# Kernel optimization log

Measured on AMD Instinct MI355X. Metric: run time of the kernel, lower is better.

The kernel has to match this reference:

```python
import jax, jax.numpy as jnp
import numpy as np

BLANK = 0
SIZE_AVERAGE = True


def rnnt_loss(acts, labels, act_lens, label_lens):
    # acts: (B, T, U+1, V) raw logits; warp-transducer applies log_softmax internally
    B, T, U1, V = acts.shape
    U = U1 - 1
    logp = jax.nn.log_softmax(acts, axis=-1)          # (B,T,U1,V)
    lp_blank = logp[..., BLANK]                       # (B,T,U1)
    # emission log-prob of label u at grid point (t,u): logp[b,t,u,labels[b,u]]
    lp_emit = jnp.take_along_axis(
        logp[:, :, :U, :], labels[:, None, :, None].astype(jnp.int32), axis=3
    )[..., 0]                                         # (B,T,U)

    # alpha[0,0]=0 ; alpha[0,u] = sum_{k<u} emit[0,k]
    row0 = jnp.concatenate(
        [jnp.zeros((B, 1), acts.dtype), jnp.cumsum(lp_emit[:, 0, :], axis=1)], axis=1
    )                                                 # (B,U1)

    def outer(prev_row, xs):
        blank_prev, emit_t = xs                       # (B,U1), (B,U)
        fb = prev_row + blank_prev                    # arrive via blank from t-1
        def inner(carry, x):
            fb_u, em_prev = x                         # (B,), (B,)
            a = jnp.logaddexp(fb_u, carry + em_prev)  # blank vs emit path
            return a, a
        _, rest = jax.lax.scan(inner, fb[:, 0], (fb[:, 1:].T, emit_t.T))  # (U,B)
        row = jnp.concatenate([fb[:, :1], rest.T], axis=1)               # (B,U1)
        return row, row

    xs = (jnp.moveaxis(lp_blank[:, :-1, :], 1, 0),   # (T-1,B,U1)
          jnp.moveaxis(lp_emit[:, 1:, :], 1, 0))     # (T-1,B,U)
    _, rows = jax.lax.scan(outer, row0, xs)          # (T-1,B,U1)
    alpha = jnp.concatenate([row0[None], rows], axis=0)  # (T,B,U1)

    b_idx = jnp.arange(B)
    t_idx = act_lens.astype(jnp.int32) - 1
    u_idx = label_lens.astype(jnp.int32)
    loglike = alpha[t_idx, b_idx, u_idx] + lp_blank[b_idx, t_idx, u_idx]
    total = -jnp.sum(loglike)
    if SIZE_AVERAGE:
        total = total / B
    return total.reshape(1)


def setup_inputs() -> dict:
    key = jax.random.key(0)
    k1, k2, k3, k4 = jax.random.split(key, 4)
    B, T, U, V = 8, 256, 100, 128
    acts = jax.random.normal(k1, (B, T, U + 1, V), dtype=jnp.float32)
    labels = jax.random.randint(k2, (B, U), 0, V, dtype=jnp.int64)
    act_lens = jax.random.randint(k3, (B,), T // 2, T + 1, dtype=jnp.int32)
    label_lens = jax.random.randint(k4, (B,), U // 2, U + 1, dtype=jnp.int32)
    return {"acts": acts, "labels": labels, "act_lens": act_lens, "label_lens": label_lens}


def reference(acts, labels, act_lens, label_lens):
    return rnnt_loss(acts, labels, act_lens, label_lens)
```

## Files before the change

### kernel.cpp

```cpp
#include <hip/hip_runtime.h>
#include <math.h>


#define B_DIM  8
#define T_DIM  256
#define U_DIM  100
#define U1_DIM 101
#define V_DIM  128

#define ROWU   128
#define DROWS  360
#define NEGF   (-8.0e29f)
#define LOG2E  1.4426950408889634f
#define LN2    0.69314718055994530942f

#define NITMAX 88
#define VROWU  320
#define DEPTH  16

typedef unsigned uv2 __attribute__((ext_vector_type(2)));

__device__ __forceinline__ float ubit(unsigned u) { return __builtin_bit_cast(float, u); }
__device__ __forceinline__ float logadd2(float a, float b) {
    float m = fmaxf(a, b);
    float e = exp2f(-fabsf(a - b));
    return m + log2f(1.0f + e);
}
__device__ __forceinline__ float lse3(float a, float b, float c) {
    float m = fmaxf(fmaxf(a, b), c);
    float s = exp2f(a - m) + exp2f(b - m) + exp2f(c - m);
    return m + log2f(s);
}
__device__ __forceinline__ float lse5(float a, float b, float c, float d, float e) {
    float m = fmaxf(fmaxf(fmaxf(a, b), c), fmaxf(d, e));
    float s = exp2f(a - m) + exp2f(b - m) + exp2f(c - m) + exp2f(d - m) + exp2f(e - m);
    return m + log2f(s);
}
__device__ __forceinline__ float lane_shr1(float x) {
    int r = __builtin_amdgcn_update_dpp(0, __builtin_bit_cast(int, x),
                                        0x138 , 0xF, 0xF, true);
    return __builtin_bit_cast(float, r);
}
__device__ __forceinline__ unsigned f2bf(float f) {
    unsigned u = __builtin_bit_cast(unsigned, f);
    u += 0x7FFF + ((u >> 16) & 1);
    return u >> 16;
}

struct W2 { float tA, mA, lA, tB, mB, lB; };
__device__ __forceinline__ W2 buildW2m(uv2 c0, uv2 cm, int l, int d, int tl, int ul) {
    const int ua = 2 * l, ub = 2 * l + 1;
    float BL0a = ubit(c0.x << 16), EM0a = ubit(c0.x & 0xFFFF0000u);
    float BL0b = ubit(c0.y << 16), EM0b = ubit(c0.y & 0xFFFF0000u);
    float BLma = ubit(cm.x << 16), EMma = ubit(cm.x & 0xFFFF0000u);
    float BLmb = ubit(cm.y << 16), EMmb = ubit(cm.y & 0xFFFF0000u);
    BL0a = (ua <= ul && (unsigned)(d - 1 - ua) <= (unsigned)tl) ? BL0a : NEGF;
    BL0b = (ub <= ul && (unsigned)(d - 1 - ub) <= (unsigned)tl) ? BL0b : NEGF;
    EM0a = (ua >= 1 && ua <= ul && (unsigned)(d - ua) <= (unsigned)tl) ? EM0a : NEGF;
    EM0b = (ub <= ul && (unsigned)(d - ub) <= (unsigned)tl) ? EM0b : NEGF;
    BLma = (ua <= ul && (unsigned)(d - 2 - ua) <= (unsigned)tl) ? BLma : NEGF;
    BLmb = (ub <= ul && (unsigned)(d - 1 - ub) <= (unsigned)tl) ? BLmb : NEGF;
    EMma = (ua >= 1 && ua <= ul && (unsigned)(d - 1 - ua) <= (unsigned)tl) ? EMma : NEGF;
    EMmb = (ub <= ul && (unsigned)(d - 1 - ub) <= (unsigned)tl) ? EMmb : NEGF;
    float BLmp = lane_shr1(BLmb), EMmp = lane_shr1(EMmb);
    W2 w;
    w.tA = BLma + BL0a;
    w.mA = logadd2(EMma + BL0a, BLmp + EM0a);
    w.lA = EMmp + EM0a;
    w.tB = BLmb + BL0b;
    w.mB = logadd2(EMmb + BL0b, BLma + EM0b);
    w.lB = EMma + EM0b;
    if (l == 0) { w.mA = NEGF; w.lA = NEGF; w.lB = NEGF; }
    return w;
}

__device__ __forceinline__ void buildV4(const unsigned* combB, int dt, int l,
                                        int tl, int ul, float* out) {
    const unsigned* C = combB + (size_t)dt * ROWU + 2 * l;
    uv2 c0 = *(const uv2*)(C);
    uv2 c1 = *(const uv2*)(C - ROWU);
    uv2 c2 = *(const uv2*)(C - 2 * ROWU);
    uv2 c3 = *(const uv2*)(C - 3 * ROWU);
    W2 P = buildW2m(c0, c1, l, dt,     tl, ul);
    W2 Q = buildW2m(c2, c3, l, dt - 2, tl, ul);
    float Qt_b1 = lane_shr1(Q.tB), Qm_b1 = lane_shr1(Q.mB), Ql_b1 = lane_shr1(Q.lB);
    float Qt_a1 = lane_shr1(Q.tA), Qm_a1 = lane_shr1(Q.mA), Ql_a1 = lane_shr1(Q.lA);
    out[0] = P.tA + Q.tA;
    out[1] = logadd2(P.tA + Q.mA, P.mA + Qt_b1);
    out[2] = lse3(P.tA + Q.lA, P.mA + Qm_b1, P.lA + Qt_a1);
    out[3] = logadd2(P.mA + Ql_b1, P.lA + Qm_a1);
    out[4] = P.lA + Ql_a1;
    out[5] = P.tB + Q.tB;
    out[6] = logadd2(P.tB + Q.mB, P.mB + Q.tA);
    out[7] = lse3(P.tB + Q.lB, P.mB + Q.mA, P.lB + Qt_b1);
    out[8] = logadd2(P.mB + Q.lA, P.lB + Qm_b1);
    out[9] = P.lB + Ql_b1;
    if (l == 0) { out[1] = NEGF; out[2] = NEGF; out[3] = NEGF; out[4] = NEGF; }
}

__device__ __forceinline__ void prologue(const unsigned* combB, int start, int l,
                                         int tl, int ul, float& v0, float& v1) {
    v0 = (l == 0) ? 0.0f : NEGF;
    v1 = NEGF;
    for (int d = 1; d <= start; ++d) {
        uv2 c = *(const uv2*)(combB + (size_t)d * ROWU + 2 * l);
        const int ua = 2 * l, ub = 2 * l + 1;
        float bl0 = ubit(c.x << 16), em0 = ubit(c.x & 0xFFFF0000u);
        float bl1 = ubit(c.y << 16), em1 = ubit(c.y & 0xFFFF0000u);
        bl0 = (ua <= ul && (unsigned)(d - 1 - ua) <= (unsigned)tl) ? bl0 : NEGF;
        bl1 = (ub <= ul && (unsigned)(d - 1 - ub) <= (unsigned)tl) ? bl1 : NEGF;
        em0 = (ua >= 1 && ua <= ul && (unsigned)(d - ua) <= (unsigned)tl) ? em0 : NEGF;
        em1 = (ub <= ul && (unsigned)(d - ub) <= (unsigned)tl) ? em1 : NEGF;
        float left0 = lane_shr1(v1);
        float a0 = v0 + bl0, p0 = left0 + em0;
        float a1 = v1 + bl1, p1 = v0 + em1;
        v0 = logadd2(a0, p0);
        v1 = logadd2(a1, p1);
    }
}

__global__ __launch_bounds__(256) void lsm_kernel(
    const float* __restrict__ acts, const int* __restrict__ labels,
    const int* __restrict__ act_lens, const int* __restrict__ label_lens,
    unsigned short* __restrict__ comb, int* __restrict__ counter, int nrows)
{
    if (blockIdx.x == 0 && threadIdx.x == 0) *counter = 0;

    int rid = blockIdx.x * 8 + (threadIdx.x >> 5);
    if (rid >= nrows) return;
    int hl = threadIdx.x & 31;

    int u  = rid % U1_DIM;
    int bt = rid / U1_DIM;
    int b  = bt / T_DIM;
    int t  = bt - b * T_DIM;
    if (t >= act_lens[b] || u > label_lens[b]) return;

    const float* row = acts + (size_t)rid * V_DIM;
    float4 x = *reinterpret_cast<const float4*>(row + 4 * hl);
    float4 y = make_float4(x.x * LOG2E, x.y * LOG2E, x.z * LOG2E, x.w * LOG2E);

    float s = exp2f(y.x) + exp2f(y.y) + exp2f(y.z) + exp2f(y.w);
    #pragma unroll
    for (int off = 16; off; off >>= 1) s += __shfl_xor(s, off);
    float lse2 = log2f(s);

    unsigned short* C = comb + (size_t)b * DROWS * (ROWU * 2);
    int d = t + u + 1;
    if (hl == 0)
        C[(size_t)d * (ROWU * 2) + 2 * u] = (unsigned short)f2bf(y.x - lse2);
    if (u < U_DIM) {
        int lab = labels[b * U_DIM + u];
        if (hl == (lab >> 2)) {
            int r = lab & 3;
            float v = (r == 0) ? y.x : (r == 1) ? y.y : (r == 2) ? y.z : y.w;
            C[(size_t)d * (ROWU * 2) + 2 * u + 3] = (unsigned short)f2bf(v - lse2);
        }
    }
}

__global__ __launch_bounds__(256) void v4c_kernel(
    const unsigned* __restrict__ comb,
    const int* __restrict__ act_lens, const int* __restrict__ label_lens,
    unsigned* __restrict__ V)
{
    int wid = blockIdx.x * 4 + (threadIdx.x >> 6);
    if (wid >= B_DIM * NITMAX) return;
    int l  = threadIdx.x & 63;
    int b  = wid / NITMAX;
    int it = wid - b * NITMAX;

    int tl = act_lens[b] - 1, ul = label_lens[b];
    int dfin = tl + ul, start = dfin & 3, niter = dfin >> 2;
    if (it >= niter) return;
    int dt = start + 4 * (it + 1);

    float o[10];
    buildV4(comb + (size_t)b * DROWS * ROWU, dt, l, tl, ul, o);

    if (l < 52) {
        unsigned* ro = V + (size_t)(b * NITMAX + it) * VROWU;
        uv2 p0, p1, p2;
        p0.x = f2bf(o[0]) | (f2bf(o[1]) << 16); p0.y = f2bf(o[5]) | (f2bf(o[6]) << 16);
        p1.x = f2bf(o[2]) | (f2bf(o[3]) << 16); p1.y = f2bf(o[7]) | (f2bf(o[8]) << 16);
        p2.x = f2bf(o[4]);                      p2.y = f2bf(o[9]);
        __builtin_nontemporal_store(p0, (uv2*)(ro + 2 * l));
        __builtin_nontemporal_store(p1, (uv2*)(ro + 104 + 2 * l));
        __builtin_nontemporal_store(p2, (uv2*)(ro + 208 + 2 * l));
    }
}

__global__ __launch_bounds__(64, 1) void dp3_kernel(
    const unsigned* __restrict__ comb, const unsigned* __restrict__ V,
    const int* __restrict__ act_lens, const int* __restrict__ label_lens,
    float* __restrict__ loglike, int* __restrict__ counter,
    float* __restrict__ out)
{
    const int b = blockIdx.x;
    const int l = threadIdx.x;
    const int tl    = act_lens[b] - 1;
    const int ul    = label_lens[b];
    const int dfin  = tl + ul;
    const int start = dfin & 3;
    const int niter = dfin >> 2;

    const unsigned* combB = comb + (size_t)b * DROWS * ROWU;
    const char* Vc = (const char*)(V + (size_t)b * NITMAX * VROWU) + 8 * l;

    float fin_bl = ubit(combB[(size_t)(dfin + 1) * ROWU + ul] << 16);
    float v0, v1;
    prologue(combB, start, l, tl, ul, v0, v1);
    float rf0 = NEGF, rf1 = NEGF;

    asm volatile("s_waitcnt vmcnt(0)" ::: "memory");

    uv2 r0[DEPTH], r1[DEPTH], r2[DEPTH];
    #pragma unroll
    for (int j = 0; j < DEPTH; ++j) {
        const char* p = Vc + (size_t)j * (VROWU * 4);
        asm volatile("global_load_dwordx2 %0, %1, off" : "=v"(r0[j]) : "v"(p));
        asm volatile("global_load_dwordx2 %0, %1, off" : "=v"(r1[j]) : "v"(p + 416));
        asm volatile("global_load_dwordx2 %0, %1, off" : "=v"(r2[j]) : "v"(p + 832));
    }
    const int ngroups = (niter + DEPTH - 1) / DEPTH;
    for (int g = 0; g < ngroups; ++g) {
        const int it0 = g * DEPTH;
        #pragma unroll
        for (int q = 0; q < 4; ++q) {
            asm volatile("s_waitcnt vmcnt(36)");
            __builtin_amdgcn_sched_barrier(0);
            #pragma unroll
            for (int j4 = 0; j4 < 4; ++j4) {
                const int J = q * 4 + j4;
                const int it = it0 + J;
                uv2 a0 = r0[J], a1 = r1[J], a2 = r2[J];
                float V0a = ubit(a0.x << 16), V1a = ubit(a0.x & 0xFFFF0000u);
                float V0b = ubit(a0.y << 16), V1b = ubit(a0.y & 0xFFFF0000u);
                float V2a = ubit(a1.x << 16), V3a = ubit(a1.x & 0xFFFF0000u);
                float V2b = ubit(a1.y << 16), V3b = ubit(a1.y & 0xFFFF0000u);
                float V4a = ubit(a2.x << 16), V4b = ubit(a2.y << 16);
                float s1 = lane_shr1(v1);
                float s0 = lane_shr1(v0);
                float s3 = lane_shr1(s1);
                float s2 = lane_shr1(s0);
                float nA = lse5(v0 + V0a, s1 + V1a, s0 + V2a, s3 + V3a, s2 + V4a);
                float nB = lse5(v1 + V0b, v0 + V1b, s1 + V2b, s0 + V3b, s3 + V4b);
                if (it == niter - 1) { rf0 = nA; rf1 = nB; }
                v0 = nA; v1 = nB;
                int rr = it + DEPTH; rr = rr < NITMAX ? rr : NITMAX - 1;
                const char* p = Vc + (size_t)rr * (VROWU * 4);
                asm volatile("global_load_dwordx2 %0, %1, off" : "=v"(r0[J]) : "v"(p));
                asm volatile("global_load_dwordx2 %0, %1, off" : "=v"(r1[J]) : "v"(p + 416));
                asm volatile("global_load_dwordx2 %0, %1, off" : "=v"(r2[J]) : "v"(p + 832));
            }
        }
    }

    float res = (ul & 1) ? rf1 : rf0;
    if (l == (ul >> 1)) {
        loglike[b] = LN2 * (res + fin_bl);
        __threadfence();
        int old = atomicAdd(counter, 1);
        if (old == B_DIM - 1) {
            __threadfence();
            float s = 0.0f;
            #pragma unroll
            for (int i = 0; i < B_DIM; ++i)
                s += __hip_atomic_load(&loglike[i], __ATOMIC_RELAXED,
                                       __HIP_MEMORY_SCOPE_AGENT);
            out[0] = -s / (float)B_DIM;
        }
    }
}

extern "C" void kernel_launch(void* const* d_in, const int* in_sizes, int n_in,
                              void* d_out, int out_size, void* d_ws, size_t ws_size,
                              hipStream_t stream) {
    const float* acts       = (const float*)d_in[0];
    const int*   labels     = (const int*)d_in[1];
    const int*   act_lens   = (const int*)d_in[2];
    const int*   label_lens = (const int*)d_in[3];

    unsigned* comb    = (unsigned*)d_ws;
    unsigned* V       = comb + (size_t)B_DIM * DROWS * ROWU;
    float*    loglike = (float*)(V + (size_t)B_DIM * NITMAX * VROWU);
    int*      counter = (int*)(loglike + B_DIM);

    int nrows   = B_DIM * T_DIM * U1_DIM;
    int nblocks = (nrows + 7) / 8;

    lsm_kernel<<<nblocks, 256, 0, stream>>>(acts, labels, act_lens, label_lens,
                                            (unsigned short*)comb, counter, nrows);
    int vwaves = B_DIM * NITMAX;
    v4c_kernel<<<(vwaves + 3) / 4, 256, 0, stream>>>(comb, act_lens, label_lens, V);
    dp3_kernel<<<B_DIM, 64, 0, stream>>>(comb, V, act_lens, label_lens,
                                         loglike, counter, (float*)d_out);
}
```

Baseline: 51.64 us.

## Stage per-batch V table into LDS before the serial DP loop

```diff
diff --git a/kernel.cpp b/kernel.cpp
--- a/kernel.cpp
+++ b/kernel.cpp
@@ -16,7 +16,8 @@
 
 #define NITMAX 88
 #define VROWU  320
-#define DEPTH  16
+#define VROWB  1280
+#define LDS_BYTES (NITMAX * VROWB)
 
 typedef unsigned uv2 __attribute__((ext_vector_type(2)));
 
@@ -196,6 +197,8 @@
     float* __restrict__ loglike, int* __restrict__ counter,
     float* __restrict__ out)
 {
+    extern __shared__ char sV[];
+
     const int b = blockIdx.x;
     const int l = threadIdx.x;
     const int tl    = act_lens[b] - 1;
@@ -205,54 +208,58 @@
     const int niter = dfin >> 2;
 
     const unsigned* combB = comb + (size_t)b * DROWS * ROWU;
-    const char* Vc = (const char*)(V + (size_t)b * NITMAX * VROWU) + 8 * l;
 
     float fin_bl = ubit(combB[(size_t)(dfin + 1) * ROWU + ul] << 16);
     float v0, v1;
     prologue(combB, start, l, tl, ul, v0, v1);
+    asm volatile("s_waitcnt vmcnt(0)" ::: "memory");
+
+    {
+        const char* g = (const char*)(V + (size_t)b * NITMAX * VROWU) + l * 16;
+        const int nload = (niter * VROWB + 1023) >> 10;
+        for (int i = 0; i < nload; ++i) {
+            __builtin_amdgcn_global_load_lds(
+                (const __attribute__((address_space(1))) void*)(g + (size_t)i * 1024),
+                (__attribute__((address_space(3))) void*)(sV + (size_t)i * 1024), 16, 0, 0);
+        }
+        asm volatile("s_waitcnt vmcnt(0)" ::: "memory");
+    }
+
     float rf0 = NEGF, rf1 = NEGF;
-
-    asm volatile("s_waitcnt vmcnt(0)" ::: "memory");
-
-    uv2 r0[DEPTH], r1[DEPTH], r2[DEPTH];
+    const char* Lc = sV + 8 * l;
+    uv2 q0[4], q1[4], q2[4];
     #pragma unroll
-    for (int j = 0; j < DEPTH; ++j) {
-        const char* p = Vc + (size_t)j * (VROWU * 4);
-        asm volatile("global_load_dwordx2 %0, %1, off" : "=v"(r0[j]) : "v"(p));
-        asm volatile("global_load_dwordx2 %0, %1, off" : "=v"(r1[j]) : "v"(p + 416));
-        asm volatile("global_load_dwordx2 %0, %1, off" : "=v"(r2[j]) : "v"(p + 832));
-    }
-    const int ngroups = (niter + DEPTH - 1) / DEPTH;
-    for (int g = 0; g < ngroups; ++g) {
-        const int it0 = g * DEPTH;
+    for (int j = 0; j < 4; ++j) {
+        const char* p = Lc + (size_t)j * VROWB;
+        q0[j] = *(const uv2*)(p);
+        q1[j] = *(const uv2*)(p + 416);
+        q2[j] = *(const uv2*)(p + 832);
+    }
+    const int ngroups = (niter + 3) >> 2;
+    for (int g4 = 0; g4 < ngroups; ++g4) {
+        const int it0 = g4 * 4;
         #pragma unroll
-        for (int q = 0; q < 4; ++q) {
-            asm volatile("s_waitcnt vmcnt(36)");
-            __builtin_amdgcn_sched_barrier(0);
-            #pragma unroll
-            for (int j4 = 0; j4 < 4; ++j4) {
-                const int J = q * 4 + j4;
-                const int it = it0 + J;
-                uv2 a0 = r0[J], a1 = r1[J], a2 = r2[J];
-                float V0a = ubit(a0.x << 16), V1a = ubit(a0.x & 0xFFFF0000u);
-                float V0b = ubit(a0.y << 16), V1b = ubit(a0.y & 0xFFFF0000u);
-                float V2a = ubit(a1.x << 16), V3a = ubit(a1.x & 0xFFFF0000u);
-                float V2b = ubit(a1.y << 16), V3b = ubit(a1.y & 0xFFFF0000u);
-                float V4a = ubit(a2.x << 16), V4b = ubit(a2.y << 16);
-                float s1 = lane_shr1(v1);
-                float s0 = lane_shr1(v0);
-                float s3 = lane_shr1(s1);
-                float s2 = lane_shr1(s0);
-                float nA = lse5(v0 + V0a, s1 + V1a, s0 + V2a, s3 + V3a, s2 + V4a);
-                float nB = lse5(v1 + V0b, v0 + V1b, s1 + V2b, s0 + V3b, s3 + V4b);
-                if (it == niter - 1) { rf0 = nA; rf1 = nB; }
-                v0 = nA; v1 = nB;
-                int rr = it + DEPTH; rr = rr < NITMAX ? rr : NITMAX - 1;
-                const char* p = Vc + (size_t)rr * (VROWU * 4);
-                asm volatile("global_load_dwordx2 %0, %1, off" : "=v"(r0[J]) : "v"(p));
-                asm volatile("global_load_dwordx2 %0, %1, off" : "=v"(r1[J]) : "v"(p + 416));
-                asm volatile("global_load_dwordx2 %0, %1, off" : "=v"(r2[J]) : "v"(p + 832));
-            }
+        for (int J = 0; J < 4; ++J) {
+            const int it = it0 + J;
+            uv2 a0 = q0[J], a1 = q1[J], a2 = q2[J];
+            float V0a = ubit(a0.x << 16), V1a = ubit(a0.x & 0xFFFF0000u);
+            float V0b = ubit(a0.y << 16), V1b = ubit(a0.y & 0xFFFF0000u);
+            float V2a = ubit(a1.x << 16), V3a = ubit(a1.x & 0xFFFF0000u);
+            float V2b = ubit(a1.y << 16), V3b = ubit(a1.y & 0xFFFF0000u);
+            float V4a = ubit(a2.x << 16), V4b = ubit(a2.y << 16);
+            float s1 = lane_shr1(v1);
+            float s0 = lane_shr1(v0);
+            float s3 = lane_shr1(s1);
+            float s2 = lane_shr1(s0);
+            float nA = lse5(v0 + V0a, s1 + V1a, s0 + V2a, s3 + V3a, s2 + V4a);
+            float nB = lse5(v1 + V0b, v0 + V1b, s1 + V2b, s0 + V3b, s3 + V4b);
+            if (it == niter - 1) { rf0 = nA; rf1 = nB; }
+            v0 = nA; v1 = nB;
+            int rr = it + 4; rr = rr < niter ? rr : niter - 1;
+            const char* p = Lc + (size_t)rr * VROWB;
+            q0[J] = *(const uv2*)(p);
+            q1[J] = *(const uv2*)(p + 416);
+            q2[J] = *(const uv2*)(p + 832);
         }
     }
 
@@ -289,10 +296,13 @@
     int nrows   = B_DIM * T_DIM * U1_DIM;
     int nblocks = (nrows + 7) / 8;
 
+    hipFuncSetAttribute(reinterpret_cast<const void*>(dp3_kernel),
+                        hipFuncAttributeMaxDynamicSharedMemorySize, LDS_BYTES);
+
     lsm_kernel<<<nblocks, 256, 0, stream>>>(acts, labels, act_lens, label_lens,
                                             (unsigned short*)comb, counter, nrows);
     int vwaves = B_DIM * NITMAX;
     v4c_kernel<<<(vwaves + 3) / 4, 256, 0, stream>>>(comb, act_lens, label_lens, V);
-    dp3_kernel<<<B_DIM, 64, 0, stream>>>(comb, V, act_lens, label_lens,
-                                         loglike, counter, (float*)d_out);
-}
+    dp3_kernel<<<B_DIM, 64, LDS_BYTES, stream>>>(comb, V, act_lens, label_lens,
+                                                 loglike, counter, (float*)d_out);
+}
```

After: 49.56 us (median of 2 runs). 4.0% less time.
